# Optimization experiments

Hardware: AMD Instinct MI355X
Metric: run time of the kernel (lower is better)

Reference implementation:

```python
import jax, jax.numpy as jnp
import numpy as np
import math

B, N, H, D = 2, 2048, 16, 64

def setup_inputs() -> dict:
    key = jax.random.key(0)
    kq, kk, kv = jax.random.split(key, 3)
    q = jax.random.normal(kq, (B, N, H, D), dtype=jnp.float32)
    k = jax.random.normal(kk, (B, N, H, D), dtype=jnp.float32)
    v = jax.random.normal(kv, (B, N, H, D), dtype=jnp.float32)
    return {"q": q, "k": k, "v": v}

def reference(q, k, v):
    d = q.shape[-1]
    # [b,n,h,d] -> [b,h,n,d]
    qh = jnp.transpose(q, (0, 2, 1, 3))
    kh = jnp.transpose(k, (0, 2, 1, 3))
    vh = jnp.transpose(v, (0, 2, 1, 3))
    # scores: [b,h,n,n]
    scores = jnp.einsum('bhqd,bhkd->bhqk', qh, kh) / math.sqrt(d)
    # jax.nn.softmax performs the stable max-subtraction internally,
    # matching the original's explicit max-subtract + softmax.
    attn = jax.nn.softmax(scores, axis=-1)
    o = jnp.einsum('bhqk,bhkd->bhqd', attn, vh)
    # back to [b,n,h,d]
    return jnp.transpose(o, (0, 2, 1, 3))
```

## Files before the change

kernel.cpp:

```cpp
#include <hip/hip_runtime.h>


typedef float  f32x4  __attribute__((ext_vector_type(4)));
typedef float  f32x16 __attribute__((ext_vector_type(16)));
typedef short  s16x8  __attribute__((ext_vector_type(8)));
typedef short  s16x4  __attribute__((ext_vector_type(4)));
typedef int    i32x4  __attribute__((ext_vector_type(4)));

#define QSCALE 0.18033688011112042f

__device__ __forceinline__ unsigned short bf16r(float f) {
    unsigned u = __builtin_bit_cast(unsigned, f);
    u += 0x7fffu + ((u >> 16) & 1u);
    return (unsigned short)(u >> 16);
}

__device__ __forceinline__ s16x8 cvt8f_scaled(const float* p, float s) {
    f32x4 a = *(const f32x4*)p;
    f32x4 b = *(const f32x4*)(p + 4);
    s16x8 r;
#pragma unroll
    for (int i = 0; i < 4; ++i) {
        r[i]   = (short)bf16r(a[i] * s);
        r[i+4] = (short)bf16r(b[i] * s);
    }
    return r;
}

__device__ __forceinline__ int cvtpk2(float lo, float hi) {
    int r;
    asm("v_cvt_pk_bf16_f32 %0, %1, %2" : "=v"(r) : "v"(lo), "v"(hi));
    return r;
}

__global__ void __launch_bounds__(256)
prep(const float* __restrict__ K, const float* __restrict__ V,
     unsigned short* __restrict__ Kt, unsigned short* __restrict__ Vt) {
    const int t = threadIdx.x, bid = blockIdx.x;
    const int bh = bid & 31, nb = bid >> 5;
    const int b = bh >> 4, h = bh & 15;
    const size_t tile0 = ((size_t)bh * 64 + nb * 2) * 2048;

#pragma unroll
    for (int i = 0; i < 2; ++i) {
        const int lin = i * 256 + t;
        const int kbl = lin >> 8, rem = lin & 255;
        const int kc = rem >> 6, l = rem & 63;
        const int nl = l & 31, gg = l >> 5;
        const float* src = K + ((size_t)(b * 2048 + nb * 64 + kbl * 32 + nl)) * 1024
                             + h * 64 + kc * 16 + gg * 8;
        f32x4 a = *(const f32x4*)src;
        f32x4 c = *(const f32x4*)(src + 4);
        i32x4 o = { cvtpk2(a[0], a[1]), cvtpk2(a[2], a[3]),
                    cvtpk2(c[0], c[1]), cvtpk2(c[2], c[3]) };
        *(i32x4*)(Kt + tile0 + kbl * 2048 + kc * 512 + l * 8) = o;
    }

#pragma unroll
    for (int i = 0; i < 2; ++i) {
        const int lin = i * 256 + t;
        const int kbl = lin >> 8, rem = lin & 255;
        const int qq = rem >> 6, l = rem & 63;
        const int dt = qq >> 1, s = qq & 1;
        const int nl = l & 31, gg = l >> 5;
        const float* vp0 = V + ((size_t)(b * 2048 + nb * 64 + kbl * 32 + 8 * s + 4 * gg)) * 1024
                             + h * 64 + dt * 32 + nl;
        float x0 = vp0[0],     x1 = vp0[1024],  x2 = vp0[2048],  x3 = vp0[3072];
        float x4 = vp0[16384], x5 = vp0[17408], x6 = vp0[18432], x7 = vp0[19456];
        i32x4 o = { cvtpk2(x0, x1), cvtpk2(x2, x3),
                    cvtpk2(x4, x5), cvtpk2(x6, x7) };
        *(i32x4*)(Vt + tile0 + kbl * 2048 + qq * 512 + l * 8) = o;
    }
}

__global__ void __launch_bounds__(256, 2)
attn_fwd(const float* __restrict__ Q, const unsigned short* __restrict__ Kt,
         const unsigned short* __restrict__ Vt, float* __restrict__ O)
{
    __shared__ __align__(16) float ex[2 * 64 * 68];

    const int t = threadIdx.x;
    const int w = t >> 6, lane = t & 63;
    const int g = lane >> 5, nl = lane & 31;
    const int qsel = w & 1, ksel = w >> 1;

    const int bid = blockIdx.x;
    const int bh  = bid & 31, qb = bid >> 5;
    const int b   = bh >> 4,  h  = bh & 15;
    const int q0  = qb * 128 + qsel * 64;

    s16x8 qf[2][4];
#pragma unroll
    for (int qt = 0; qt < 2; ++qt) {
        const float* qp = Q + ((size_t)(b * 2048 + q0 + qt * 32 + nl)) * 1024
                            + h * 64 + g * 8;
#pragma unroll
        for (int kc = 0; kc < 4; ++kc)
            qf[qt][kc] = cvt8f_scaled(qp + kc * 16, QSCALE);
    }

    const unsigned short* ka = Kt + (size_t)bh * 131072 + (size_t)ksel * 65536 + lane * 8;
    const unsigned short* va = Vt + (size_t)bh * 131072 + (size_t)ksel * 65536 + lane * 8;

    f32x16 oa00 = {}, oa01 = {}, oa10 = {}, oa11 = {};
    f32x4  lpv0 = {}, lpv1 = {};

    s16x8 kfa[4], vfa[4], kfb[4], vfb[4];

#define LOADT(KD, VD) do {                                                  \
        _Pragma("unroll")                                                   \
        for (int _i = 0; _i < 4; ++_i) {                                    \
            KD[_i] = *(const s16x8*)(ka + _i * 512);                        \
            VD[_i] = *(const s16x8*)(va + _i * 512);                        \
        }                                                                   \
        ka += 2048; va += 2048; } while (0)

#define QKROW(KF, QFq, LPV, PK) do {                                        \
        f32x16 sacc = {};                                                   \
        _Pragma("unroll")                                                   \
        for (int _kc = 0; _kc < 4; ++_kc)                                   \
            sacc = __builtin_amdgcn_mfma_f32_32x32x16_bf16(                 \
                KF[_kc], QFq[_kc], sacc, 0, 0, 0);                          \
        _Pragma("unroll")                                                   \
        for (int _c = 0; _c < 4; ++_c) {                                    \
            f32x4 e = { __builtin_amdgcn_exp2f(sacc[4*_c]),                 \
                        __builtin_amdgcn_exp2f(sacc[4*_c+1]),               \
                        __builtin_amdgcn_exp2f(sacc[4*_c+2]),               \
                        __builtin_amdgcn_exp2f(sacc[4*_c+3]) };             \
            LPV += e;                                                       \
            PK[2*_c]   = cvtpk2(e[0], e[1]);                                \
            PK[2*_c+1] = cvtpk2(e[2], e[3]);                                \
        } } while (0)

#define STEP(KF, VF) do {                                                   \
        int pk0[8], pk1[8];                                                 \
        QKROW(KF, qf[0], lpv0, pk0);                                        \
        QKROW(KF, qf[1], lpv1, pk1);                                        \
        _Pragma("unroll")                                                   \
        for (int _s = 0; _s < 2; ++_s) {                                    \
            i32x4 b0 = { pk0[_s*2], pk0[_s*2+1], pk0[_s*2+4], pk0[_s*2+5] };\
            i32x4 b1 = { pk1[_s*2], pk1[_s*2+1], pk1[_s*2+4], pk1[_s*2+5] };\
            s16x8 bb0 = __builtin_bit_cast(s16x8, b0);                      \
            s16x8 bb1 = __builtin_bit_cast(s16x8, b1);                      \
            oa00 = __builtin_amdgcn_mfma_f32_32x32x16_bf16(VF[_s],     bb0, oa00, 0, 0, 0); \
            oa10 = __builtin_amdgcn_mfma_f32_32x32x16_bf16(VF[2 + _s], bb0, oa10, 0, 0, 0); \
            oa01 = __builtin_amdgcn_mfma_f32_32x32x16_bf16(VF[_s],     bb1, oa01, 0, 0, 0); \
            oa11 = __builtin_amdgcn_mfma_f32_32x32x16_bf16(VF[2 + _s], bb1, oa11, 0, 0, 0); \
        } } while (0)

    LOADT(kfa, vfa);
    LOADT(kfb, vfb);

    for (int n = 0; n < 15; ++n) {
        __builtin_amdgcn_sched_barrier(0);
        STEP(kfa, vfa);
        LOADT(kfa, vfa);
        __builtin_amdgcn_sched_barrier(0);
        STEP(kfb, vfb);
        LOADT(kfb, vfb);
    }
    __builtin_amdgcn_sched_barrier(0);
    STEP(kfa, vfa);
    STEP(kfb, vfb);

#undef LOADT
#undef QKROW
#undef STEP

    float lp[2] = { lpv0[0] + lpv0[1] + lpv0[2] + lpv0[3],
                    lpv1[0] + lpv1[1] + lpv1[2] + lpv1[3] };

    __syncthreads();
    float* zone = ex + qsel * (64 * 68) + lane * 68;
    if (ksel) {
#pragma unroll
        for (int i = 0; i < 4; ++i) {
            *(f32x4*)(zone + i * 4) =
                (f32x4){ oa00[4*i], oa00[4*i+1], oa00[4*i+2], oa00[4*i+3] };
            *(f32x4*)(zone + 16 + i * 4) =
                (f32x4){ oa01[4*i], oa01[4*i+1], oa01[4*i+2], oa01[4*i+3] };
            *(f32x4*)(zone + 32 + i * 4) =
                (f32x4){ oa10[4*i], oa10[4*i+1], oa10[4*i+2], oa10[4*i+3] };
            *(f32x4*)(zone + 48 + i * 4) =
                (f32x4){ oa11[4*i], oa11[4*i+1], oa11[4*i+2], oa11[4*i+3] };
        }
        zone[64] = lp[0];
        zone[65] = lp[1];
    }
    __syncthreads();
    if (!ksel) {
#pragma unroll
        for (int i = 0; i < 4; ++i) {
            f32x4 u0 = *(const f32x4*)(zone + i * 4);
            f32x4 u1 = *(const f32x4*)(zone + 16 + i * 4);
            f32x4 u2 = *(const f32x4*)(zone + 32 + i * 4);
            f32x4 u3 = *(const f32x4*)(zone + 48 + i * 4);
#pragma unroll
            for (int j = 0; j < 4; ++j) {
                oa00[4*i+j] += u0[j]; oa01[4*i+j] += u1[j];
                oa10[4*i+j] += u2[j]; oa11[4*i+j] += u3[j];
            }
        }
        float inv[2];
#pragma unroll
        for (int qt = 0; qt < 2; ++qt) {
            float s = lp[qt] + zone[64 + qt];
            s += __shfl_xor(s, 32);
            inv[qt] = 1.0f / s;
        }
        float* op0 = O + ((size_t)(b * 2048 + q0 + nl)) * 1024 + h * 64;
        float* op1 = op0 + 32 * 1024;
#pragma unroll
        for (int rq = 0; rq < 4; ++rq) {
            const int d0 = 8 * rq + 4 * g;
            *(f32x4*)(op0 + d0) = (f32x4){
                oa00[4*rq]   * inv[0], oa00[4*rq+1] * inv[0],
                oa00[4*rq+2] * inv[0], oa00[4*rq+3] * inv[0] };
            *(f32x4*)(op0 + 32 + d0) = (f32x4){
                oa10[4*rq]   * inv[0], oa10[4*rq+1] * inv[0],
                oa10[4*rq+2] * inv[0], oa10[4*rq+3] * inv[0] };
            *(f32x4*)(op1 + d0) = (f32x4){
                oa01[4*rq]   * inv[1], oa01[4*rq+1] * inv[1],
                oa01[4*rq+2] * inv[1], oa01[4*rq+3] * inv[1] };
            *(f32x4*)(op1 + 32 + d0) = (f32x4){
                oa11[4*rq]   * inv[1], oa11[4*rq+1] * inv[1],
                oa11[4*rq+2] * inv[1], oa11[4*rq+3] * inv[1] };
        }
    }
}

extern "C" void kernel_launch(void* const* d_in, const int* in_sizes, int n_in,
                              void* d_out, int out_size, void* d_ws, size_t ws_size,
                              hipStream_t stream) {
    const float* q = (const float*)d_in[0];
    const float* k = (const float*)d_in[1];
    const float* v = (const float*)d_in[2];
    float* o = (float*)d_out;

    unsigned short* Kt = (unsigned short*)d_ws;
    unsigned short* Vt = Kt + 4194304;

    hipLaunchKernelGGL(prep,     dim3(1024), dim3(256), 0, stream, k, v, Kt, Vt);
    hipLaunchKernelGGL(attn_fwd, dim3(512),  dim3(256), 0, stream, q, Kt, Vt, o);
}
```

Baseline: 127.5 us.

## Split keys four ways per block and stream K/V tiles through LDS

Each block now handles 64 queries, and its four waves each cover a quarter of the key range, so the grid doubles to 1024 blocks. K and V tiles now reach LDS through global_load_lds async copies, with explicit vmcnt and lgkmcnt waits, instead of register double-buffering. Occupancy is raised to 3 blocks per SM, and the final reduction combines three partial accumulators through shared memory. The goal is more parallelism and less register pressure. The cost is extra LDS round trips, a serialising wait after each tile, and a larger cross-wave reduction.

```diff
diff --git a/kernel.cpp b/kernel.cpp
--- a/kernel.cpp
+++ b/kernel.cpp
@@ -31,6 +31,12 @@
     int r;
     asm("v_cvt_pk_bf16_f32 %0, %1, %2" : "=v"(r) : "v"(lo), "v"(hi));
     return r;
+}
+
+__device__ __forceinline__ void gll16(const unsigned short* g, short* l) {
+    __builtin_amdgcn_global_load_lds(
+        (const __attribute__((address_space(1))) unsigned int*)g,
+        (__attribute__((address_space(3))) unsigned int*)l, 16, 0, 0);
 }
 
 __global__ void __launch_bounds__(256)
@@ -73,21 +79,20 @@
     }
 }
 
-__global__ void __launch_bounds__(256, 2)
+__global__ void __launch_bounds__(256, 3)
 attn_fwd(const float* __restrict__ Q, const unsigned short* __restrict__ Kt,
          const unsigned short* __restrict__ Vt, float* __restrict__ O)
 {
-    __shared__ __align__(16) float ex[2 * 64 * 68];
+    __shared__ __align__(16) char smem[52224];
 
     const int t = threadIdx.x;
-    const int w = t >> 6, lane = t & 63;
+    const int ksel = t >> 6, lane = t & 63;
     const int g = lane >> 5, nl = lane & 31;
-    const int qsel = w & 1, ksel = w >> 1;
 
     const int bid = blockIdx.x;
     const int bh  = bid & 31, qb = bid >> 5;
     const int b   = bh >> 4,  h  = bh & 15;
-    const int q0  = qb * 128 + qsel * 64;
+    const int q0  = qb * 64;
 
     s16x8 qf[2][4];
 #pragma unroll
@@ -98,81 +103,97 @@
         for (int kc = 0; kc < 4; ++kc)
             qf[qt][kc] = cvt8f_scaled(qp + kc * 16, QSCALE);
     }
-
-    const unsigned short* ka = Kt + (size_t)bh * 131072 + (size_t)ksel * 65536 + lane * 8;
-    const unsigned short* va = Vt + (size_t)bh * 131072 + (size_t)ksel * 65536 + lane * 8;
+    asm volatile("s_waitcnt vmcnt(0)" ::: "memory");
+    __builtin_amdgcn_sched_barrier(0);
+
+    const unsigned short* gk = Kt + (size_t)bh * 131072 + (size_t)ksel * 32768 + lane * 8;
+    const unsigned short* gv = Vt + (size_t)bh * 131072 + (size_t)ksel * 32768 + lane * 8;
+
+    short* sK = (short*)(smem + ksel * 8192);
+    short* sV = (short*)(smem + ksel * 8192 + 4096);
 
     f32x16 oa00 = {}, oa01 = {}, oa10 = {}, oa11 = {};
     f32x4  lpv0 = {}, lpv1 = {};
 
-    s16x8 kfa[4], vfa[4], kfb[4], vfb[4];
-
-#define LOADT(KD, VD) do {                                                  \
+#define ISSUEK(IT) do { const unsigned short* _g = gk + (IT) * 2048;        \
         _Pragma("unroll")                                                   \
-        for (int _i = 0; _i < 4; ++_i) {                                    \
-            KD[_i] = *(const s16x8*)(ka + _i * 512);                        \
-            VD[_i] = *(const s16x8*)(va + _i * 512);                        \
-        }                                                                   \
-        ka += 2048; va += 2048; } while (0)
-
-#define QKROW(KF, QFq, LPV, PK) do {                                        \
-        f32x16 sacc = {};                                                   \
+        for (int _i = 0; _i < 4; ++_i) gll16(_g + _i * 512, sK + _i * 512); \
+        } while (0)
+#define ISSUEV(IT) do { const unsigned short* _g = gv + (IT) * 2048;        \
         _Pragma("unroll")                                                   \
-        for (int _kc = 0; _kc < 4; ++_kc)                                   \
-            sacc = __builtin_amdgcn_mfma_f32_32x32x16_bf16(                 \
-                KF[_kc], QFq[_kc], sacc, 0, 0, 0);                          \
-        _Pragma("unroll")                                                   \
-        for (int _c = 0; _c < 4; ++_c) {                                    \
-            f32x4 e = { __builtin_amdgcn_exp2f(sacc[4*_c]),                 \
-                        __builtin_amdgcn_exp2f(sacc[4*_c+1]),               \
-                        __builtin_amdgcn_exp2f(sacc[4*_c+2]),               \
-                        __builtin_amdgcn_exp2f(sacc[4*_c+3]) };             \
-            LPV += e;                                                       \
-            PK[2*_c]   = cvtpk2(e[0], e[1]);                                \
-            PK[2*_c+1] = cvtpk2(e[2], e[3]);                                \
-        } } while (0)
-
-#define STEP(KF, VF) do {                                                   \
-        int pk0[8], pk1[8];                                                 \
-        QKROW(KF, qf[0], lpv0, pk0);                                        \
-        QKROW(KF, qf[1], lpv1, pk1);                                        \
-        _Pragma("unroll")                                                   \
-        for (int _s = 0; _s < 2; ++_s) {                                    \
-            i32x4 b0 = { pk0[_s*2], pk0[_s*2+1], pk0[_s*2+4], pk0[_s*2+5] };\
-            i32x4 b1 = { pk1[_s*2], pk1[_s*2+1], pk1[_s*2+4], pk1[_s*2+5] };\
-            s16x8 bb0 = __builtin_bit_cast(s16x8, b0);                      \
-            s16x8 bb1 = __builtin_bit_cast(s16x8, b1);                      \
-            oa00 = __builtin_amdgcn_mfma_f32_32x32x16_bf16(VF[_s],     bb0, oa00, 0, 0, 0); \
-            oa10 = __builtin_amdgcn_mfma_f32_32x32x16_bf16(VF[2 + _s], bb0, oa10, 0, 0, 0); \
-            oa01 = __builtin_amdgcn_mfma_f32_32x32x16_bf16(VF[_s],     bb1, oa01, 0, 0, 0); \
-            oa11 = __builtin_amdgcn_mfma_f32_32x32x16_bf16(VF[2 + _s], bb1, oa11, 0, 0, 0); \
-        } } while (0)
-
-    LOADT(kfa, vfa);
-    LOADT(kfb, vfb);
-
-    for (int n = 0; n < 15; ++n) {
-        __builtin_amdgcn_sched_barrier(0);
-        STEP(kfa, vfa);
-        LOADT(kfa, vfa);
-        __builtin_amdgcn_sched_barrier(0);
-        STEP(kfb, vfb);
-        LOADT(kfb, vfb);
-    }
-    __builtin_amdgcn_sched_barrier(0);
-    STEP(kfa, vfa);
-    STEP(kfb, vfb);
-
-#undef LOADT
-#undef QKROW
-#undef STEP
+        for (int _i = 0; _i < 4; ++_i) gll16(_g + _i * 512, sV + _i * 512); \
+        } while (0)
+#define WAITV(N) do {                                                       \
+        asm volatile("s_waitcnt vmcnt(" #N ")" ::: "memory");               \
+        __builtin_amdgcn_sched_barrier(0); } while (0)
+#define LGKM0 do {                                                          \
+        asm volatile("s_waitcnt lgkmcnt(0)" ::: "memory");                  \
+        __builtin_amdgcn_sched_barrier(0); } while (0)
+
+    ISSUEK(0);
+    ISSUEV(0);
+
+#pragma unroll
+    for (int it = 0; it < 16; ++it) {
+        WAITV(4);
+        s16x8 kf[4];
+#pragma unroll
+        for (int kc = 0; kc < 4; ++kc)
+            kf[kc] = *(const s16x8*)&sK[kc * 512 + lane * 8];
+        LGKM0;
+        if (it < 15) ISSUEK(it + 1);
+
+        f32x16 s0 = {}, s1 = {};
+#pragma unroll
+        for (int kc = 0; kc < 4; ++kc) {
+            s0 = __builtin_amdgcn_mfma_f32_32x32x16_bf16(kf[kc], qf[0][kc], s0, 0, 0, 0);
+            s1 = __builtin_amdgcn_mfma_f32_32x32x16_bf16(kf[kc], qf[1][kc], s1, 0, 0, 0);
+        }
+        int pk0[8], pk1[8];
+#pragma unroll
+        for (int c = 0; c < 4; ++c) {
+            f32x4 e0 = { __builtin_amdgcn_exp2f(s0[4*c]),   __builtin_amdgcn_exp2f(s0[4*c+1]),
+                         __builtin_amdgcn_exp2f(s0[4*c+2]), __builtin_amdgcn_exp2f(s0[4*c+3]) };
+            f32x4 e1 = { __builtin_amdgcn_exp2f(s1[4*c]),   __builtin_amdgcn_exp2f(s1[4*c+1]),
+                         __builtin_amdgcn_exp2f(s1[4*c+2]), __builtin_amdgcn_exp2f(s1[4*c+3]) };
+            lpv0 += e0; lpv1 += e1;
+            pk0[2*c]   = cvtpk2(e0[0], e0[1]);  pk0[2*c+1] = cvtpk2(e0[2], e0[3]);
+            pk1[2*c]   = cvtpk2(e1[0], e1[1]);  pk1[2*c+1] = cvtpk2(e1[2], e1[3]);
+        }
+
+        if (it < 15) { WAITV(4); } else { WAITV(0); }
+        s16x8 vf[4];
+#pragma unroll
+        for (int qq = 0; qq < 4; ++qq)
+            vf[qq] = *(const s16x8*)&sV[qq * 512 + lane * 8];
+        LGKM0;
+        if (it < 15) ISSUEV(it + 1);
+
+#pragma unroll
+        for (int s = 0; s < 2; ++s) {
+            i32x4 b0 = { pk0[s*2], pk0[s*2+1], pk0[s*2+4], pk0[s*2+5] };
+            i32x4 b1 = { pk1[s*2], pk1[s*2+1], pk1[s*2+4], pk1[s*2+5] };
+            s16x8 bb0 = __builtin_bit_cast(s16x8, b0);
+            s16x8 bb1 = __builtin_bit_cast(s16x8, b1);
+            oa00 = __builtin_amdgcn_mfma_f32_32x32x16_bf16(vf[s],     bb0, oa00, 0, 0, 0);
+            oa10 = __builtin_amdgcn_mfma_f32_32x32x16_bf16(vf[2 + s], bb0, oa10, 0, 0, 0);
+            oa01 = __builtin_amdgcn_mfma_f32_32x32x16_bf16(vf[s],     bb1, oa01, 0, 0, 0);
+            oa11 = __builtin_amdgcn_mfma_f32_32x32x16_bf16(vf[2 + s], bb1, oa11, 0, 0, 0);
+        }
+    }
+
+#undef ISSUEK
+#undef ISSUEV
+#undef WAITV
+#undef LGKM0
 
     float lp[2] = { lpv0[0] + lpv0[1] + lpv0[2] + lpv0[3],
                     lpv1[0] + lpv1[1] + lpv1[2] + lpv1[3] };
 
     __syncthreads();
-    float* zone = ex + qsel * (64 * 68) + lane * 68;
+    float* ex = (float*)smem;
     if (ksel) {
+        float* zone = ex + (ksel - 1) * (64 * 68) + lane * 68;
 #pragma unroll
         for (int i = 0; i < 4; ++i) {
             *(f32x4*)(zone + i * 4) =
@@ -189,24 +210,31 @@
     }
     __syncthreads();
     if (!ksel) {
-#pragma unroll
-        for (int i = 0; i < 4; ++i) {
-            f32x4 u0 = *(const f32x4*)(zone + i * 4);
-            f32x4 u1 = *(const f32x4*)(zone + 16 + i * 4);
-            f32x4 u2 = *(const f32x4*)(zone + 32 + i * 4);
-            f32x4 u3 = *(const f32x4*)(zone + 48 + i * 4);
-#pragma unroll
-            for (int j = 0; j < 4; ++j) {
-                oa00[4*i+j] += u0[j]; oa01[4*i+j] += u1[j];
-                oa10[4*i+j] += u2[j]; oa11[4*i+j] += u3[j];
+        float lps0 = lp[0], lps1 = lp[1];
+#pragma unroll
+        for (int z = 0; z < 3; ++z) {
+            const float* zn = ex + z * (64 * 68) + lane * 68;
+#pragma unroll
+            for (int i = 0; i < 4; ++i) {
+                f32x4 u0 = *(const f32x4*)(zn + i * 4);
+                f32x4 u1 = *(const f32x4*)(zn + 16 + i * 4);
+                f32x4 u2 = *(const f32x4*)(zn + 32 + i * 4);
+                f32x4 u3 = *(const f32x4*)(zn + 48 + i * 4);
+#pragma unroll
+                for (int j = 0; j < 4; ++j) {
+                    oa00[4*i+j] += u0[j]; oa01[4*i+j] += u1[j];
+                    oa10[4*i+j] += u2[j]; oa11[4*i+j] += u3[j];
+                }
             }
+            lps0 += zn[64];
+            lps1 += zn[65];
         }
         float inv[2];
-#pragma unroll
-        for (int qt = 0; qt < 2; ++qt) {
-            float s = lp[qt] + zone[64 + qt];
-            s += __shfl_xor(s, 32);
-            inv[qt] = 1.0f / s;
+        {
+            float ss0 = lps0 + __shfl_xor(lps0, 32);
+            float ss1 = lps1 + __shfl_xor(lps1, 32);
+            inv[0] = 1.0f / ss0;
+            inv[1] = 1.0f / ss1;
         }
         float* op0 = O + ((size_t)(b * 2048 + q0 + nl)) * 1024 + h * 64;
         float* op1 = op0 + 32 * 1024;
@@ -241,5 +269,5 @@
     unsigned short* Vt = Kt + 4194304;
 
     hipLaunchKernelGGL(prep,     dim3(1024), dim3(256), 0, stream, k, v, Kt, Vt);
-    hipLaunchKernelGGL(attn_fwd, dim3(512),  dim3(256), 0, stream, q, Kt, Vt, o);
-}
+    hipLaunchKernelGGL(attn_fwd, dim3(1024), dim3(256), 0, stream, q, Kt, Vt, o);
+}
```

After: 132.9 us. 4.2% more time.

## Software-pipeline QK MFMA with exp/PV across query halves, single-buffer K/V

Applied to the files above, without the earlier changes.

Restructures the inner attention loop so the QK MFMA chain for one query half overlaps the exp2/packing and PV MFMAs of the other half. K/V go from double-buffered register tiles to a single buffer refilled mid-iteration, and s_setprio is raised around the MFMA chains. The aim is to hide transcendental and conversion latency behind matrix work and to free registers. The cost is less load prefetch distance, which can expose global/L2 latency, since the K refill is consumed in the very next QK chain.

```diff
diff --git a/kernel.cpp b/kernel.cpp
--- a/kernel.cpp
+++ b/kernel.cpp
@@ -99,73 +99,90 @@
             qf[qt][kc] = cvt8f_scaled(qp + kc * 16, QSCALE);
     }
 
-    const unsigned short* ka = Kt + (size_t)bh * 131072 + (size_t)ksel * 65536 + lane * 8;
-    const unsigned short* va = Vt + (size_t)bh * 131072 + (size_t)ksel * 65536 + lane * 8;
+    const unsigned short* kp = Kt + (size_t)bh * 131072 + (size_t)ksel * 65536 + lane * 8;
+    const unsigned short* vp = Vt + (size_t)bh * 131072 + (size_t)ksel * 65536 + lane * 8;
 
     f32x16 oa00 = {}, oa01 = {}, oa10 = {}, oa11 = {};
+    f32x16 sE, sO;
     f32x4  lpv0 = {}, lpv1 = {};
 
-    s16x8 kfa[4], vfa[4], kfb[4], vfb[4];
-
-#define LOADT(KD, VD) do {                                                  \
-        _Pragma("unroll")                                                   \
-        for (int _i = 0; _i < 4; ++_i) {                                    \
-            KD[_i] = *(const s16x8*)(ka + _i * 512);                        \
-            VD[_i] = *(const s16x8*)(va + _i * 512);                        \
-        }                                                                   \
-        ka += 2048; va += 2048; } while (0)
-
-#define QKROW(KF, QFq, LPV, PK) do {                                        \
-        f32x16 sacc = {};                                                   \
+    s16x8 kf[4], vf[4];
+
+#define QKCHAIN(DST, QFq) do {                                              \
+        DST = (f32x16){};                                                   \
+        __builtin_amdgcn_s_setprio(1);                                      \
         _Pragma("unroll")                                                   \
         for (int _kc = 0; _kc < 4; ++_kc)                                   \
-            sacc = __builtin_amdgcn_mfma_f32_32x32x16_bf16(                 \
-                KF[_kc], QFq[_kc], sacc, 0, 0, 0);                          \
+            DST = __builtin_amdgcn_mfma_f32_32x32x16_bf16(                  \
+                kf[_kc], QFq[_kc], DST, 0, 0, 0);                           \
+        __builtin_amdgcn_s_setprio(0); } while (0)
+
+#define EXPPK1(S, LPV, PK) do {                                             \
         _Pragma("unroll")                                                   \
         for (int _c = 0; _c < 4; ++_c) {                                    \
-            f32x4 e = { __builtin_amdgcn_exp2f(sacc[4*_c]),                 \
-                        __builtin_amdgcn_exp2f(sacc[4*_c+1]),               \
-                        __builtin_amdgcn_exp2f(sacc[4*_c+2]),               \
-                        __builtin_amdgcn_exp2f(sacc[4*_c+3]) };             \
+            f32x4 e = { __builtin_amdgcn_exp2f(S[4*_c]),                    \
+                        __builtin_amdgcn_exp2f(S[4*_c+1]),                  \
+                        __builtin_amdgcn_exp2f(S[4*_c+2]),                  \
+                        __builtin_amdgcn_exp2f(S[4*_c+3]) };                \
             LPV += e;                                                       \
             PK[2*_c]   = cvtpk2(e[0], e[1]);                                \
             PK[2*_c+1] = cvtpk2(e[2], e[3]);                                \
         } } while (0)
 
-#define STEP(KF, VF) do {                                                   \
-        int pk0[8], pk1[8];                                                 \
-        QKROW(KF, qf[0], lpv0, pk0);                                        \
-        QKROW(KF, qf[1], lpv1, pk1);                                        \
+#define PVQ(PK, OA0, OA1) do {                                              \
+        __builtin_amdgcn_s_setprio(1);                                      \
         _Pragma("unroll")                                                   \
         for (int _s = 0; _s < 2; ++_s) {                                    \
-            i32x4 b0 = { pk0[_s*2], pk0[_s*2+1], pk0[_s*2+4], pk0[_s*2+5] };\
-            i32x4 b1 = { pk1[_s*2], pk1[_s*2+1], pk1[_s*2+4], pk1[_s*2+5] };\
-            s16x8 bb0 = __builtin_bit_cast(s16x8, b0);                      \
-            s16x8 bb1 = __builtin_bit_cast(s16x8, b1);                      \
-            oa00 = __builtin_amdgcn_mfma_f32_32x32x16_bf16(VF[_s],     bb0, oa00, 0, 0, 0); \
-            oa10 = __builtin_amdgcn_mfma_f32_32x32x16_bf16(VF[2 + _s], bb0, oa10, 0, 0, 0); \
-            oa01 = __builtin_amdgcn_mfma_f32_32x32x16_bf16(VF[_s],     bb1, oa01, 0, 0, 0); \
-            oa11 = __builtin_amdgcn_mfma_f32_32x32x16_bf16(VF[2 + _s], bb1, oa11, 0, 0, 0); \
-        } } while (0)
-
-    LOADT(kfa, vfa);
-    LOADT(kfb, vfb);
-
-    for (int n = 0; n < 15; ++n) {
-        __builtin_amdgcn_sched_barrier(0);
-        STEP(kfa, vfa);
-        LOADT(kfa, vfa);
-        __builtin_amdgcn_sched_barrier(0);
-        STEP(kfb, vfb);
-        LOADT(kfb, vfb);
-    }
-    __builtin_amdgcn_sched_barrier(0);
-    STEP(kfa, vfa);
-    STEP(kfb, vfb);
-
-#undef LOADT
-#undef QKROW
-#undef STEP
+            i32x4 bd = { PK[_s*2], PK[_s*2+1], PK[_s*2+4], PK[_s*2+5] };    \
+            s16x8 bb = __builtin_bit_cast(s16x8, bd);                       \
+            OA0 = __builtin_amdgcn_mfma_f32_32x32x16_bf16(vf[_s],     bb, OA0, 0, 0, 0); \
+            OA1 = __builtin_amdgcn_mfma_f32_32x32x16_bf16(vf[2 + _s], bb, OA1, 0, 0, 0); \
+        }                                                                   \
+        __builtin_amdgcn_s_setprio(0); } while (0)
+
+#define REFILL_K do {                                                       \
+        _Pragma("unroll")                                                   \
+        for (int _i = 0; _i < 4; ++_i)                                      \
+            kf[_i] = *(const s16x8*)(kp + _i * 512); } while (0)
+#define REFILL_V do {                                                       \
+        _Pragma("unroll")                                                   \
+        for (int _i = 0; _i < 4; ++_i)                                      \
+            vf[_i] = *(const s16x8*)(vp + _i * 512); } while (0)
+
+    REFILL_K;
+    REFILL_V;
+    kp += 2048;
+    vp += 2048;
+    QKCHAIN(sE, qf[0]);
+
+#pragma unroll 1
+    for (int m = 0; m < 31; ++m) {
+        int pk[8];
+        QKCHAIN(sO, qf[1]);
+        REFILL_K;
+        kp += 2048;
+        EXPPK1(sE, lpv0, pk);
+        PVQ(pk, oa00, oa10);
+        QKCHAIN(sE, qf[0]);
+        EXPPK1(sO, lpv1, pk);
+        PVQ(pk, oa01, oa11);
+        REFILL_V;
+        vp += 2048;
+    }
+    {
+        int pk[8];
+        QKCHAIN(sO, qf[1]);
+        EXPPK1(sE, lpv0, pk);
+        PVQ(pk, oa00, oa10);
+        EXPPK1(sO, lpv1, pk);
+        PVQ(pk, oa01, oa11);
+    }
+
+#undef QKCHAIN
+#undef EXPPK1
+#undef PVQ
+#undef REFILL_K
+#undef REFILL_V
 
     float lp[2] = { lpv0[0] + lpv0[1] + lpv0[2] + lpv0[3],
                     lpv1[0] + lpv1[1] + lpv1[2] + lpv1[3] };
```

New measurement: 128.9 us. No clear change (+1.1%).
